# Kernel optimization log

Measured on AMD Instinct MI355X. Metric: run time of the kernel, lower is better.

Reference implementation:

```python
import jax, jax.numpy as jnp
import numpy as np

B, S, H = 32, 512, 2048
FP, SP = 1024, 1024


def setup_inputs() -> dict:
    key = jax.random.key(0)
    ks = jax.random.split(key, 8)
    X = jax.random.normal(ks[0], (B, S, H), dtype=jnp.float32)
    pY = jax.random.randint(ks[1], (B, S), 0, 3)
    # Y must be consistent with pY: hcw rows index [2, 2+FP), roo rows [2+FP, 2+FP+SP)
    y_hcw = jax.random.randint(ks[2], (B, S), 2, 2 + FP)
    y_roo = jax.random.randint(ks[3], (B, S), 2 + FP, 2 + FP + SP)
    Y = jnp.where(pY == 1, y_hcw, jnp.where(pY == 2, y_roo, 0))
    sc = 1.0 / np.sqrt(H)
    W_end = jax.random.normal(ks[4], (1, H), dtype=jnp.float32) * sc
    b_end = jnp.zeros((1,), jnp.float32)
    W_hcw = jax.random.normal(ks[5], (FP, H), dtype=jnp.float32) * sc
    b_hcw = jnp.zeros((FP,), jnp.float32)
    W_roo = jax.random.normal(ks[6], (SP, H), dtype=jnp.float32) * sc
    b_roo = jnp.zeros((SP,), jnp.float32)
    return {"X": X, "pY": pY, "Y": Y, "W_end": W_end, "b_end": b_end,
            "W_hcw": W_hcw, "b_hcw": b_hcw, "W_roo": W_roo, "b_roo": b_roo}


def reference(X, pY, Y, W_end, b_end, W_hcw, b_hcw, W_roo, b_roo):
    b, s, h = X.shape
    N = b * s
    Xf = X.reshape(N, h)
    pYf = pY.reshape(N)
    Yf = Y.reshape(N)

    end_mask = pYf == 0
    hcw_mask = pYf == 1
    roo_mask = pYf == 2

    # end head (Bernoulli prob)
    end_logit = Xf @ W_end.T + b_end            # [N, 1]
    end_prob = jax.nn.sigmoid(end_logit)[:, 0]  # [N]
    non_end = 1.0 - end_prob

    # hcw / roo heads: dense compute over all tokens, masked results match
    # the torch gather/scatter exactly at valid positions.
    P_hcw = jax.nn.softmax(Xf @ W_hcw.T + b_hcw, axis=-1)  # [N, FP]
    P_roo = jax.nn.softmax(Xf @ W_roo.T + b_roo, axis=-1)  # [N, SP]

    fp = W_hcw.shape[0]
    sp = W_roo.shape[0]
    idx_hcw = jnp.clip(Yf - 2, 0, fp - 1)
    idx_roo = jnp.clip(Yf - 2 - fp, 0, sp - 1)
    prob_hcw = jnp.take_along_axis(P_hcw, idx_hcw[:, None], axis=1)[:, 0]
    prob_roo = jnp.take_along_axis(P_roo, idx_roo[:, None], axis=1)[:, 0]

    prob = jnp.where(end_mask, end_prob,
                     jnp.where(hcw_mask, prob_hcw * non_end,
                               jnp.where(roo_mask, prob_roo * non_end, 1.0)))

    em = end_mask.astype(X.dtype)[:, None]
    hm = hcw_mask.astype(X.dtype)[:, None]
    rm = roo_mask.astype(X.dtype)[:, None]
    col_end = jnp.broadcast_to(end_prob[:, None], (N, 2)) * em        # [N, 2]
    col_hcw = P_hcw * non_end[:, None] * hm                           # [N, FP]
    col_roo = P_roo * non_end[:, None] * rm                           # [N, SP]
    prob_all_mat = jnp.concatenate([col_end, col_hcw, col_roo], axis=-1)

    log_prob = jnp.log(prob)
    return log_prob.reshape(b, s), prob_all_mat.reshape(b, s, fp + sp + 2)
```

## Files before the change

### kernel.cpp

```cpp
#include <hip/hip_runtime.h>
#include <hip/hip_bf16.h>
#include <cstddef>
#include <cstdint>

#define N_TOK 16384
#define H_    2048
#define FP_   1024
#define SP_   1024
#define C_    2050

#define BM 128
#define BN 128
#define BK 64
#define KP 72

typedef short bf16x8 __attribute__((ext_vector_type(8)));
typedef float f32x4  __attribute__((ext_vector_type(4)));

__device__ __forceinline__ unsigned pack_bf2(float a, float b) {
  __hip_bfloat16 x = __float2bfloat16(a);
  __hip_bfloat16 y = __float2bfloat16(b);
  unsigned short ux, uy;
  __builtin_memcpy(&ux, &x, 2);
  __builtin_memcpy(&uy, &y, 2);
  return (unsigned)ux | ((unsigned)uy << 16);
}

__device__ __forceinline__ unsigned short f2bf(float f) {
  __hip_bfloat16 h = __float2bfloat16(f);
  unsigned short u;
  __builtin_memcpy(&u, &h, 2);
  return u;
}

__device__ __forceinline__ float bf2f(unsigned short u) {
  unsigned v = (unsigned)u << 16;
  float f;
  __builtin_memcpy(&f, &v, 4);
  return f;
}

__global__ __launch_bounds__(256) void convert_kernel(
    const float* __restrict__ X,
    const float* __restrict__ W_hcw, const float* __restrict__ W_roo,
    const float* __restrict__ W_end, const float* __restrict__ b_end,
    unsigned short* __restrict__ Xb, unsigned short* __restrict__ Wb,
    float* __restrict__ mat)
{
  const int wave = threadIdx.x >> 6;
  const int lane = threadIdx.x & 63;
  const int row  = (blockIdx.x << 2) + wave;
  const bool isX = row < N_TOK;
  const float* src;
  unsigned short* dst;
  if (isX) {
    src = X + (size_t)row * H_;
    dst = Xb + (size_t)row * H_;
  } else {
    const int m = row - N_TOK;
    src = (m < FP_) ? (W_hcw + (size_t)m * H_) : (W_roo + (size_t)(m - FP_) * H_);
    dst = Wb + (size_t)m * H_;
  }
  float s = 0.f;
#pragma unroll
  for (int i = 0; i < 8; ++i) {
    const int e = (lane << 2) + (i << 8);
    float4 v = *(const float4*)(src + e);
    uint2 p;
    p.x = pack_bf2(v.x, v.y);
    p.y = pack_bf2(v.z, v.w);
    *(uint2*)(dst + e) = p;
    if (isX) {
      float4 w = *(const float4*)(W_end + e);
      s += v.x * w.x + v.y * w.y + v.z * w.z + v.w * w.w;
    }
  }
  if (isX) {
#pragma unroll
    for (int o = 32; o; o >>= 1) s += __shfl_xor(s, o);
    if (lane == 0) mat[(size_t)row * C_] = s + b_end[0];
  }
}

__global__ __launch_bounds__(256) void gemm_lds_kernel(
    const unsigned short* __restrict__ Xb, const unsigned short* __restrict__ Wb,
    const float* __restrict__ b_hcw, const float* __restrict__ b_roo,
    float* __restrict__ mat)
{
  __shared__ __align__(16) unsigned short As[BM * BK];
  __shared__ __align__(16) unsigned short Bs[BN * BK];

  const int c0 = blockIdx.x * BN;
  const int n0 = blockIdx.y * BM;
  const float* bias = (c0 < FP_) ? (b_hcw + c0) : (b_roo + (c0 - FP_));

  const int t    = threadIdx.x;
  const int wave = t >> 6;
  const int lane = t & 63;
  const int wy   = wave >> 1;
  const int wx   = wave & 1;
  const int quad = lane >> 4;
  const int l16  = lane & 15;

  const int srow   = t >> 3;
  const int gchunk = (t & 7) ^ (srow & 7);
  const unsigned short* gA = Xb + (size_t)(n0 + srow) * H_ + (gchunk << 3);
  const unsigned short* gB = Wb + (size_t)(c0 + srow) * H_ + (gchunk << 3);

  f32x4 acc[4][4];
#pragma unroll
  for (int i = 0; i < 4; ++i)
#pragma unroll
    for (int j = 0; j < 4; ++j)
#pragma unroll
      for (int r = 0; r < 4; ++r) acc[i][j][r] = 0.f;

  for (int k0 = 0; k0 < H_; k0 += BK) {
#pragma unroll
    for (int r = 0; r < 4; ++r) {
      __builtin_amdgcn_global_load_lds(
          (const __attribute__((address_space(1))) unsigned int*)(gA + (size_t)(r * 32) * H_ + k0),
          (__attribute__((address_space(3))) unsigned int*)(&As[(r * 32 + srow) * BK + ((t & 7) << 3)]),
          16, 0, 0);
      __builtin_amdgcn_global_load_lds(
          (const __attribute__((address_space(1))) unsigned int*)(gB + (size_t)(r * 32) * H_ + k0),
          (__attribute__((address_space(3))) unsigned int*)(&Bs[(r * 32 + srow) * BK + ((t & 7) << 3)]),
          16, 0, 0);
    }
    __syncthreads();

#pragma unroll
    for (int kk = 0; kk < 2; ++kk) {
      bf16x8 af[4], bfr[4];
      const int sw = l16 & 7;
#pragma unroll
      for (int i = 0; i < 4; ++i) {
        const int pos = ((kk << 2) + quad) ^ sw;
        af[i] = *(const bf16x8*)&As[(wy * 64 + i * 16 + l16) * BK + (pos << 3)];
      }
#pragma unroll
      for (int j = 0; j < 4; ++j) {
        const int pos = ((kk << 2) + quad) ^ sw;
        bfr[j] = *(const bf16x8*)&Bs[(wx * 64 + j * 16 + l16) * BK + (pos << 3)];
      }
#pragma unroll
      for (int i = 0; i < 4; ++i)
#pragma unroll
        for (int j = 0; j < 4; ++j)
          acc[i][j] = __builtin_amdgcn_mfma_f32_16x16x32_bf16(af[i], bfr[j], acc[i][j], 0, 0, 0);
    }
    __syncthreads();
  }

  float bj[4];
#pragma unroll
  for (int j = 0; j < 4; ++j) bj[j] = bias[wx * 64 + j * 16 + l16];
#pragma unroll
  for (int i = 0; i < 4; ++i) {
#pragma unroll
    for (int r = 0; r < 4; ++r) {
      const int row = n0 + wy * 64 + i * 16 + quad * 4 + r;
      unsigned short* dst =
          (unsigned short*)(mat + (size_t)row * C_ + 4) + c0 + wx * 64 + l16;
#pragma unroll
      for (int j = 0; j < 4; ++j) dst[j * 16] = f2bf(acc[i][j][r] + bj[j]);
    }
  }
}

__global__ __launch_bounds__(256) void end_head_kernel(
    const float* __restrict__ X, const float* __restrict__ W_end,
    const float* __restrict__ b_end, float* __restrict__ mat)
{
  const int wave = threadIdx.x >> 6;
  const int lane = threadIdx.x & 63;
  const int n = (blockIdx.x << 2) + wave;
  const float* x = X + (size_t)n * H_;
  float s = 0.f;
#pragma unroll
  for (int i = 0; i < 8; ++i) {
    const int e = (lane + (i << 6)) << 2;
    float4 xv = *(const float4*)(x + e);
    float4 wv = *(const float4*)(W_end + e);
    s += xv.x * wv.x + xv.y * wv.y + xv.z * wv.z + xv.w * wv.w;
  }
#pragma unroll
  for (int o = 32; o; o >>= 1) s += __shfl_xor(s, o);
  if (lane == 0) mat[(size_t)n * C_] = s + b_end[0];
}

__global__ __launch_bounds__(256) void logits_gemm_fused(
    const float* __restrict__ X,
    const float* __restrict__ W_hcw, const float* __restrict__ W_roo,
    const float* __restrict__ b_hcw, const float* __restrict__ b_roo,
    float* __restrict__ mat)
{
  __shared__ __align__(16) unsigned short As[BM * KP];
  __shared__ __align__(16) unsigned short Bs[BN * KP];

  const int c0 = blockIdx.x * BN;
  const int n0 = blockIdx.y * BM;
  const float* Wbase = (c0 < FP_) ? (W_hcw + (size_t)c0 * H_)
                                  : (W_roo + (size_t)(c0 - FP_) * H_);
  const float* bias  = (c0 < FP_) ? (b_hcw + c0) : (b_roo + (c0 - FP_));

  const int t    = threadIdx.x;
  const int wave = t >> 6;
  const int lane = t & 63;
  const int wy   = wave >> 1;
  const int wx   = wave & 1;
  const int quad = lane >> 4;
  const int l16  = lane & 15;
  const int tq = t & 3;
  const int tr = t >> 2;

  f32x4 acc[4][4];
#pragma unroll
  for (int i = 0; i < 4; ++i)
#pragma unroll
    for (int j = 0; j < 4; ++j)
#pragma unroll
      for (int r = 0; r < 4; ++r) acc[i][j][r] = 0.f;

  for (int k0 = 0; k0 < H_; k0 += BK) {
#pragma unroll
    for (int p = 0; p < 2; ++p) {
      const int row = tr + (p << 6);
      const float4* xs = (const float4*)(X + (size_t)(n0 + row) * H_ + k0 + (tq << 4));
      const float4* ws = (const float4*)(Wbase + (size_t)row * H_ + k0 + (tq << 4));
      float4 x0 = xs[0], x1 = xs[1], x2 = xs[2], x3 = xs[3];
      float4 w0 = ws[0], w1 = ws[1], w2 = ws[2], w3 = ws[3];
      uint4 ua0 = {pack_bf2(x0.x, x0.y), pack_bf2(x0.z, x0.w),
                   pack_bf2(x1.x, x1.y), pack_bf2(x1.z, x1.w)};
      uint4 ua1 = {pack_bf2(x2.x, x2.y), pack_bf2(x2.z, x2.w),
                   pack_bf2(x3.x, x3.y), pack_bf2(x3.z, x3.w)};
      uint4 ub0 = {pack_bf2(w0.x, w0.y), pack_bf2(w0.z, w0.w),
                   pack_bf2(w1.x, w1.y), pack_bf2(w1.z, w1.w)};
      uint4 ub1 = {pack_bf2(w2.x, w2.y), pack_bf2(w2.z, w2.w),
                   pack_bf2(w3.x, w3.y), pack_bf2(w3.z, w3.w)};
      *(uint4*)&As[row * KP + (tq << 4)]     = ua0;
      *(uint4*)&As[row * KP + (tq << 4) + 8] = ua1;
      *(uint4*)&Bs[row * KP + (tq << 4)]     = ub0;
      *(uint4*)&Bs[row * KP + (tq << 4) + 8] = ub1;
    }
    __syncthreads();
#pragma unroll
    for (int kk = 0; kk < 2; ++kk) {
      bf16x8 af[4], bfr[4];
#pragma unroll
      for (int i = 0; i < 4; ++i)
        af[i] = *(const bf16x8*)&As[(wy * 64 + i * 16 + l16) * KP + kk * 32 + quad * 8];
#pragma unroll
      for (int j = 0; j < 4; ++j)
        bfr[j] = *(const bf16x8*)&Bs[(wx * 64 + j * 16 + l16) * KP + kk * 32 + quad * 8];
#pragma unroll
      for (int i = 0; i < 4; ++i)
#pragma unroll
        for (int j = 0; j < 4; ++j)
          acc[i][j] = __builtin_amdgcn_mfma_f32_16x16x32_bf16(af[i], bfr[j], acc[i][j], 0, 0, 0);
    }
    __syncthreads();
  }

  float bj[4];
#pragma unroll
  for (int j = 0; j < 4; ++j) bj[j] = bias[wx * 64 + j * 16 + l16];
#pragma unroll
  for (int i = 0; i < 4; ++i) {
#pragma unroll
    for (int r = 0; r < 4; ++r) {
      const int row = n0 + wy * 64 + i * 16 + quad * 4 + r;
      unsigned short* dst =
          (unsigned short*)(mat + (size_t)row * C_ + 4) + c0 + wx * 64 + l16;
#pragma unroll
      for (int j = 0; j < 4; ++j) dst[j * 16] = f2bf(acc[i][j][r] + bj[j]);
    }
  }
}

__global__ __launch_bounds__(256) void epilogue_kernel(
    const int* __restrict__ pY, const int* __restrict__ Yf,
    float* __restrict__ logp, float* __restrict__ mat)
{
  __shared__ float red[4];
  const int n = blockIdx.x;
  const int t = threadIdx.x;
  float* row = mat + (size_t)n * C_;
  const unsigned short* lg = (const unsigned short*)(row + 4);

  const int py = pY[n];
  const int y  = Yf[n];

  uint2 p0 = *(const uint2*)(lg + (t << 3));
  uint2 p1 = *(const uint2*)(lg + (t << 3) + 4);
  const float z = row[0];
  const int ih = min(max(y - 2, 0), FP_ - 1);
  const int ir = min(max(y - 2 - FP_, 0), SP_ - 1);
  const float lh = bf2f(lg[ih]);
  const float lr = bf2f(lg[FP_ + ir]);

  unsigned u[4] = {p0.x, p0.y, p1.x, p1.y};
  float e8[8];
  float s = 0.f;
#pragma unroll
  for (int i = 0; i < 4; ++i) {
    e8[2 * i]     = expf(bf2f((unsigned short)(u[i] & 0xffffu)));
    e8[2 * i + 1] = expf(bf2f((unsigned short)(u[i] >> 16)));
    s += e8[2 * i] + e8[2 * i + 1];
  }
#pragma unroll
  for (int o = 32; o; o >>= 1) s += __shfl_xor(s, o);
  const int w = t >> 6;
  if ((t & 63) == 0) red[w] = s;
  __syncthreads();
  const float Sh = red[0] + red[1];
  const float Sr = red[2] + red[3];

  const float sig = 1.f / (1.f + expf(-z));
  const float ne  = 1.f - sig;
  const float sc = (t < 128) ? ((py == 1) ? ne / Sh : 0.f)
                             : ((py == 2) ? ne / Sr : 0.f);
  float2* wp = (float2*)(row + 2 + (t << 3));
  wp[0] = make_float2(e8[0] * sc, e8[1] * sc);
  wp[1] = make_float2(e8[2] * sc, e8[3] * sc);
  wp[2] = make_float2(e8[4] * sc, e8[5] * sc);
  wp[3] = make_float2(e8[6] * sc, e8[7] * sc);
  if (t == 0) {
    const float ev = (py == 0) ? sig : 0.f;
    row[0] = ev;
    row[1] = ev;
    const float l1p   = log1pf(expf(-fabsf(z)));
    const float sp_z  = fmaxf(z, 0.f)  + l1p;
    const float sp_mz = fmaxf(-z, 0.f) + l1p;
    float lp;
    if      (py == 0) lp = -sp_mz;
    else if (py == 1) lp = (lh - logf(Sh)) - sp_z;
    else if (py == 2) lp = (lr - logf(Sr)) - sp_z;
    else              lp = 0.f;
    logp[n] = lp;
  }
}

extern "C" void kernel_launch(void* const* d_in, const int* in_sizes, int n_in,
                              void* d_out, int out_size, void* d_ws, size_t ws_size,
                              hipStream_t stream) {
  const float* X     = (const float*)d_in[0];
  const int*   pY    = (const int*)  d_in[1];
  const int*   Y     = (const int*)  d_in[2];
  const float* W_end = (const float*)d_in[3];
  const float* b_end = (const float*)d_in[4];
  const float* W_hcw = (const float*)d_in[5];
  const float* b_hcw = (const float*)d_in[6];
  const float* W_roo = (const float*)d_in[7];
  const float* b_roo = (const float*)d_in[8];

  float* out  = (float*)d_out;
  float* logp = out;
  float* mat  = out + N_TOK;

  const size_t xb_bytes = (size_t)N_TOK * H_ * 2;
  const size_t wb_bytes = (size_t)(FP_ + SP_) * H_ * 2;
  dim3 g(2048 / BN, N_TOK / BM);

  if (ws_size >= xb_bytes + wb_bytes) {
    unsigned short* Xb = (unsigned short*)d_ws;
    unsigned short* Wb = (unsigned short*)((char*)d_ws + xb_bytes);
    convert_kernel<<<(N_TOK + FP_ + SP_) / 4, 256, 0, stream>>>(
        X, W_hcw, W_roo, W_end, b_end, Xb, Wb, mat);
    gemm_lds_kernel<<<g, 256, 0, stream>>>(Xb, Wb, b_hcw, b_roo, mat);
  } else {
    end_head_kernel<<<N_TOK / 4, 256, 0, stream>>>(X, W_end, b_end, mat);
    logits_gemm_fused<<<g, 256, 0, stream>>>(X, W_hcw, W_roo, b_hcw, b_roo, mat);
  }
  epilogue_kernel<<<N_TOK, 256, 0, stream>>>(pY, Y, logp, mat);
}
```

Before: 433.1 us.

## Replace GEMM with 256x256 double-buffered, phased MFMA kernel with priority scheduling

Replaces the 128x128 single-buffered bf16 GEMM with a 256x256-tile, 512-thread kernel. It double-buffers LDS via global_load_lds so the next K tile is prefetched while the current one is consumed. Each K step is split into four phases of LDS fragment loads followed by MFMA bursts, separated by barriers and with raised wave priority around the math. The goal is to cut global traffic per FLOP and hide load latency, at the cost of 128KB of LDS, one block per CU, and more barriers per iteration.

Result: slower. 447.4 us (+3.3%).

```diff
diff --git a/kernel.cpp b/kernel.cpp
--- a/kernel.cpp
+++ b/kernel.cpp
@@ -82,86 +82,168 @@
   }
 }
 
-__global__ __launch_bounds__(256) void gemm_lds_kernel(
+__global__ __launch_bounds__(512) void gemm_8phase_kernel(
     const unsigned short* __restrict__ Xb, const unsigned short* __restrict__ Wb,
     const float* __restrict__ b_hcw, const float* __restrict__ b_roo,
     float* __restrict__ mat)
 {
-  __shared__ __align__(16) unsigned short As[BM * BK];
-  __shared__ __align__(16) unsigned short Bs[BN * BK];
-
-  const int c0 = blockIdx.x * BN;
-  const int n0 = blockIdx.y * BM;
+  __shared__ __align__(16) unsigned short As[2][256 * 64];
+  __shared__ __align__(16) unsigned short Bs[2][256 * 64];
+
+  const int c0 = blockIdx.x * 256;
+  const int n0 = blockIdx.y * 256;
   const float* bias = (c0 < FP_) ? (b_hcw + c0) : (b_roo + (c0 - FP_));
 
   const int t    = threadIdx.x;
   const int wave = t >> 6;
   const int lane = t & 63;
-  const int wy   = wave >> 1;
-  const int wx   = wave & 1;
+  const int wr   = wave >> 2;
+  const int wc   = wave & 3;
   const int quad = lane >> 4;
   const int l16  = lane & 15;
-
-  const int srow   = t >> 3;
-  const int gchunk = (t & 7) ^ (srow & 7);
-  const unsigned short* gA = Xb + (size_t)(n0 + srow) * H_ + (gchunk << 3);
-  const unsigned short* gB = Wb + (size_t)(c0 + srow) * H_ + (gchunk << 3);
-
-  f32x4 acc[4][4];
-#pragma unroll
-  for (int i = 0; i < 4; ++i)
-#pragma unroll
-    for (int j = 0; j < 4; ++j)
-#pragma unroll
-      for (int r = 0; r < 4; ++r) acc[i][j][r] = 0.f;
-
-  for (int k0 = 0; k0 < H_; k0 += BK) {
+  const int sw   = l16 & 7;
+
+  const int srow = t >> 3;
+  const int gch  = (t & 7) ^ (srow & 7);
+  const unsigned short* gA = Xb + (size_t)(n0 + srow) * H_ + (gch << 3);
+  const unsigned short* gB = Wb + (size_t)(c0 + srow) * H_ + (gch << 3);
+  const int lds_off = srow * 64 + ((t & 7) << 3);
+
+  auto stage = [&](int buf, int k0) {
 #pragma unroll
     for (int r = 0; r < 4; ++r) {
       __builtin_amdgcn_global_load_lds(
-          (const __attribute__((address_space(1))) unsigned int*)(gA + (size_t)(r * 32) * H_ + k0),
-          (__attribute__((address_space(3))) unsigned int*)(&As[(r * 32 + srow) * BK + ((t & 7) << 3)]),
+          (const __attribute__((address_space(1))) unsigned int*)(gA + (size_t)(r * 64) * H_ + k0),
+          (__attribute__((address_space(3))) unsigned int*)(&As[buf][r * 4096 + lds_off]),
           16, 0, 0);
       __builtin_amdgcn_global_load_lds(
-          (const __attribute__((address_space(1))) unsigned int*)(gB + (size_t)(r * 32) * H_ + k0),
-          (__attribute__((address_space(3))) unsigned int*)(&Bs[(r * 32 + srow) * BK + ((t & 7) << 3)]),
+          (const __attribute__((address_space(1))) unsigned int*)(gB + (size_t)(r * 64) * H_ + k0),
+          (__attribute__((address_space(3))) unsigned int*)(&Bs[buf][r * 4096 + lds_off]),
           16, 0, 0);
     }
-    __syncthreads();
-
-#pragma unroll
-    for (int kk = 0; kk < 2; ++kk) {
-      bf16x8 af[4], bfr[4];
-      const int sw = l16 & 7;
-#pragma unroll
-      for (int i = 0; i < 4; ++i) {
-        const int pos = ((kk << 2) + quad) ^ sw;
-        af[i] = *(const bf16x8*)&As[(wy * 64 + i * 16 + l16) * BK + (pos << 3)];
-      }
-#pragma unroll
-      for (int j = 0; j < 4; ++j) {
-        const int pos = ((kk << 2) + quad) ^ sw;
-        bfr[j] = *(const bf16x8*)&Bs[(wx * 64 + j * 16 + l16) * BK + (pos << 3)];
-      }
-#pragma unroll
-      for (int i = 0; i < 4; ++i)
-#pragma unroll
-        for (int j = 0; j < 4; ++j)
-          acc[i][j] = __builtin_amdgcn_mfma_f32_16x16x32_bf16(af[i], bfr[j], acc[i][j], 0, 0, 0);
-    }
-    __syncthreads();
+  };
+
+  f32x4 acc[8][4];
+#pragma unroll
+  for (int i = 0; i < 8; ++i)
+#pragma unroll
+    for (int j = 0; j < 4; ++j)
+#pragma unroll
+      for (int r = 0; r < 4; ++r) acc[i][j][r] = 0.f;
+
+  const int arow = wr * 128 + l16;
+  const int brow = wc * 64 + l16;
+
+  stage(0, 0);
+  stage(1, 64);
+
+  bf16x8 a[4][2], b[2][2];
+
+#pragma unroll 1
+  for (int tk = 0; tk < 32; ++tk) {
+    const int cur = tk & 1;
+    if (tk < 31) { asm volatile("s_waitcnt vmcnt(8)" ::: "memory"); }
+    else         { asm volatile("s_waitcnt vmcnt(0)" ::: "memory"); }
+    __builtin_amdgcn_sched_barrier(0);
+    __builtin_amdgcn_s_barrier();
+
+    const unsigned short* A_ = &As[cur][0];
+    const unsigned short* B_ = &Bs[cur][0];
+
+#pragma unroll
+    for (int i = 0; i < 4; ++i)
+#pragma unroll
+      for (int kk = 0; kk < 2; ++kk)
+        a[i][kk] = *(const bf16x8*)&A_[(arow + i * 16) * 64 + ((((kk << 2) + quad) ^ sw) << 3)];
+#pragma unroll
+    for (int j = 0; j < 2; ++j)
+#pragma unroll
+      for (int kk = 0; kk < 2; ++kk)
+        b[j][kk] = *(const bf16x8*)&B_[(brow + j * 16) * 64 + ((((kk << 2) + quad) ^ sw) << 3)];
+    __builtin_amdgcn_s_barrier();
+    asm volatile("s_waitcnt lgkmcnt(0)" ::: "memory");
+    __builtin_amdgcn_sched_barrier(0);
+    __builtin_amdgcn_s_setprio(1);
+#pragma unroll
+    for (int i = 0; i < 4; ++i)
+#pragma unroll
+      for (int j = 0; j < 2; ++j)
+#pragma unroll
+        for (int kk = 0; kk < 2; ++kk)
+          acc[i][j] = __builtin_amdgcn_mfma_f32_16x16x32_bf16(a[i][kk], b[j][kk], acc[i][j], 0, 0, 0);
+    __builtin_amdgcn_s_setprio(0);
+    __builtin_amdgcn_s_barrier();
+
+#pragma unroll
+    for (int j = 0; j < 2; ++j)
+#pragma unroll
+      for (int kk = 0; kk < 2; ++kk)
+        b[j][kk] = *(const bf16x8*)&B_[(brow + (j + 2) * 16) * 64 + ((((kk << 2) + quad) ^ sw) << 3)];
+    __builtin_amdgcn_s_barrier();
+    asm volatile("s_waitcnt lgkmcnt(0)" ::: "memory");
+    __builtin_amdgcn_sched_barrier(0);
+    __builtin_amdgcn_s_setprio(1);
+#pragma unroll
+    for (int i = 0; i < 4; ++i)
+#pragma unroll
+      for (int j = 0; j < 2; ++j)
+#pragma unroll
+        for (int kk = 0; kk < 2; ++kk)
+          acc[i][j + 2] = __builtin_amdgcn_mfma_f32_16x16x32_bf16(a[i][kk], b[j][kk], acc[i][j + 2], 0, 0, 0);
+    __builtin_amdgcn_s_setprio(0);
+    __builtin_amdgcn_s_barrier();
+
+#pragma unroll
+    for (int i = 0; i < 4; ++i)
+#pragma unroll
+      for (int kk = 0; kk < 2; ++kk)
+        a[i][kk] = *(const bf16x8*)&A_[(arow + (i + 4) * 16) * 64 + ((((kk << 2) + quad) ^ sw) << 3)];
+    __builtin_amdgcn_s_barrier();
+    asm volatile("s_waitcnt lgkmcnt(0)" ::: "memory");
+    __builtin_amdgcn_sched_barrier(0);
+    __builtin_amdgcn_s_setprio(1);
+#pragma unroll
+    for (int i = 0; i < 4; ++i)
+#pragma unroll
+      for (int j = 0; j < 2; ++j)
+#pragma unroll
+        for (int kk = 0; kk < 2; ++kk)
+          acc[i + 4][j + 2] = __builtin_amdgcn_mfma_f32_16x16x32_bf16(a[i][kk], b[j][kk], acc[i + 4][j + 2], 0, 0, 0);
+    __builtin_amdgcn_s_setprio(0);
+    __builtin_amdgcn_s_barrier();
+
+#pragma unroll
+    for (int j = 0; j < 2; ++j)
+#pragma unroll
+      for (int kk = 0; kk < 2; ++kk)
+        b[j][kk] = *(const bf16x8*)&B_[(brow + j * 16) * 64 + ((((kk << 2) + quad) ^ sw) << 3)];
+    __builtin_amdgcn_s_barrier();
+    asm volatile("s_waitcnt lgkmcnt(0)" ::: "memory");
+    __builtin_amdgcn_sched_barrier(0);
+    __builtin_amdgcn_s_setprio(1);
+#pragma unroll
+    for (int i = 0; i < 4; ++i)
+#pragma unroll
+      for (int j = 0; j < 2; ++j)
+#pragma unroll
+        for (int kk = 0; kk < 2; ++kk)
+          acc[i + 4][j] = __builtin_amdgcn_mfma_f32_16x16x32_bf16(a[i][kk], b[j][kk], acc[i + 4][j], 0, 0, 0);
+    __builtin_amdgcn_s_setprio(0);
+    __builtin_amdgcn_s_barrier();
+
+    if (tk < 30) stage(cur, (tk + 2) << 6);
   }
 
   float bj[4];
 #pragma unroll
-  for (int j = 0; j < 4; ++j) bj[j] = bias[wx * 64 + j * 16 + l16];
-#pragma unroll
-  for (int i = 0; i < 4; ++i) {
+  for (int j = 0; j < 4; ++j) bj[j] = bias[wc * 64 + j * 16 + l16];
+#pragma unroll
+  for (int i = 0; i < 8; ++i) {
 #pragma unroll
     for (int r = 0; r < 4; ++r) {
-      const int row = n0 + wy * 64 + i * 16 + quad * 4 + r;
+      const int row = n0 + wr * 128 + i * 16 + quad * 4 + r;
       unsigned short* dst =
-          (unsigned short*)(mat + (size_t)row * C_ + 4) + c0 + wx * 64 + l16;
+          (unsigned short*)(mat + (size_t)row * C_ + 4) + c0 + wc * 64 + l16;
 #pragma unroll
       for (int j = 0; j < 4; ++j) dst[j * 16] = f2bf(acc[i][j][r] + bj[j]);
     }
@@ -360,15 +442,16 @@
 
   const size_t xb_bytes = (size_t)N_TOK * H_ * 2;
   const size_t wb_bytes = (size_t)(FP_ + SP_) * H_ * 2;
-  dim3 g(2048 / BN, N_TOK / BM);
 
   if (ws_size >= xb_bytes + wb_bytes) {
     unsigned short* Xb = (unsigned short*)d_ws;
     unsigned short* Wb = (unsigned short*)((char*)d_ws + xb_bytes);
     convert_kernel<<<(N_TOK + FP_ + SP_) / 4, 256, 0, stream>>>(
         X, W_hcw, W_roo, W_end, b_end, Xb, Wb, mat);
-    gemm_lds_kernel<<<g, 256, 0, stream>>>(Xb, Wb, b_hcw, b_roo, mat);
+    dim3 g8(2048 / 256, N_TOK / 256);
+    gemm_8phase_kernel<<<g8, 512, 0, stream>>>(Xb, Wb, b_hcw, b_roo, mat);
   } else {
+    dim3 g(2048 / BN, N_TOK / BM);
     end_head_kernel<<<N_TOK / 4, 256, 0, stream>>>(X, W_end, b_end, mat);
     logits_gemm_fused<<<g, 256, 0, stream>>>(X, W_hcw, W_roo, b_hcw, b_roo, mat);
   }
```
